# Performance work log

Hardware: AMD Instinct MI355X
Metric: run time of the kernel (lower is better)

The kernel has to match this reference:

```python
import jax, jax.numpy as jnp
import numpy as np

NUM_HEADS = 8
NUM_GROUPS = 32
EPS = 1e-5
RESCALE = 1.0


def setup_inputs() -> dict:
    key = jax.random.key(0)
    ks = jax.random.split(key, 7)
    b, c, h, w = 16, 512, 32, 32
    return {
        "x": jax.random.normal(ks[0], (b, c, h, w), jnp.float32),
        "norm_w": jax.random.normal(ks[1], (c,), jnp.float32),
        "norm_b": jax.random.normal(ks[2], (c,), jnp.float32),
        "qkv_w": jax.random.normal(ks[3], (3 * c, c), jnp.float32) * (c ** -0.5),
        "qkv_b": jax.random.normal(ks[4], (3 * c,), jnp.float32) * 0.02,
        "proj_w": jax.random.normal(ks[5], (c, c), jnp.float32) * (c ** -0.5),
        "proj_b": jax.random.normal(ks[6], (c,), jnp.float32) * 0.02,
    }


def _group_norm(x, w, b):
    # x: [B, C, L]
    B, C, L = x.shape
    g = x.reshape(B, NUM_GROUPS, (C // NUM_GROUPS) * L)
    mu = jnp.mean(g, axis=-1, keepdims=True)
    var = jnp.var(g, axis=-1, keepdims=True)
    g = (g - mu) * jax.lax.rsqrt(var + EPS)
    return g.reshape(B, C, L) * w[None, :, None] + b[None, :, None]


def reference(x, norm_w, norm_b, qkv_w, qkv_b, proj_w, proj_b):
    b, c, hh, ww = x.shape
    L = hh * ww
    H = NUM_HEADS
    ch = c // H  # head dim

    xr = x.reshape(b, c, L)
    hid = _group_norm(xr, norm_w, norm_b)

    # 1x1 conv1d == matmul over channel dim: [3c, c] @ [b, c, L]
    qkv = jnp.einsum('oc,bcl->bol', qkv_w, hid) + qkv_b[None, :, None]
    # torch: reshape(b*H, 3*ch, L).split(ch) -> per-head contiguous [q|k|v] blocks
    qkv = qkv.reshape(b, H, 3, ch, L)
    q, k, v = qkv[:, :, 0], qkv[:, :, 1], qkv[:, :, 2]  # [b, H, ch, L]

    scale = 1.0 / (ch ** 0.25)
    weight = jnp.einsum('bhct,bhcs->bhts', q * scale, k * scale)
    weight = jax.nn.softmax(weight.astype(jnp.float32), axis=-1).astype(weight.dtype)
    a = jnp.einsum('bhts,bhcs->bhct', weight, v)  # [b, H, ch, L]

    h = a.reshape(b, c, L)
    h = jnp.einsum('oc,bcl->bol', proj_w, h) + proj_b[None, :, None]
    h = h.reshape(b, c, hh, ww)
    return (x + h) / RESCALE
```

## Files before the change

kernel.cpp:

```cpp
#include <hip/hip_runtime.h>
#include <hip/hip_bf16.h>
#include <stdint.h>


using f32x4  = __attribute__((ext_vector_type(4))) float;
using bf16x8 = __attribute__((ext_vector_type(8))) __bf16;
using s8v    = __attribute__((ext_vector_type(8))) short;
using s4v    = __attribute__((ext_vector_type(4))) short;

__device__ __forceinline__ short f2bf(float f){
  union { float f; unsigned u; } c; c.f = f;
  unsigned r = (c.u + 0x7FFFu + ((c.u >> 16) & 1u)) >> 16;
  return (short)r;
}

__device__ __forceinline__ void gl_lds16(const void* g, void* l){
  __builtin_amdgcn_global_load_lds((const __attribute__((address_space(1))) void*)g,
                                   (__attribute__((address_space(3))) void*)l, 16, 0, 0);
}

__global__ void k_convw(const float* __restrict__ qw, const float* __restrict__ pw,
                        short* __restrict__ qwb, short* __restrict__ pwb){
  int i = blockIdx.x * 256 + threadIdx.x;
  if (i < 1536*512) qwb[i] = f2bf(qw[i]);
  else              pwb[i - 1536*512] = f2bf(pw[i - 1536*512]);
}

__global__ __launch_bounds__(256) void k_gnorm(const float* __restrict__ x,
                                               const float* __restrict__ w,
                                               const float* __restrict__ bia,
                                               short* __restrict__ hid){
  int b = blockIdx.x >> 5;
  int g = blockIdx.x & 31;
  int tid = threadIdx.x;
  const float* xg = x + ((size_t)b*512 + g*16)*1024;
  int l0 = tid * 4;
  float v[16][4];
  float s1 = 0.f, s2 = 0.f;
  #pragma unroll
  for (int c = 0; c < 16; c++){
    f32x4 t = *(const f32x4*)(xg + c*1024 + l0);
    #pragma unroll
    for (int j = 0; j < 4; j++){ v[c][j] = t[j]; s1 += t[j]; s2 += t[j]*t[j]; }
  }
  #pragma unroll
  for (int m = 32; m; m >>= 1){ s1 += __shfl_xor(s1, m); s2 += __shfl_xor(s2, m); }
  __shared__ float r1[4], r2[4];
  int wv = tid >> 6, ln = tid & 63;
  if (ln == 0){ r1[wv] = s1; r2[wv] = s2; }
  __syncthreads();
  s1 = r1[0]+r1[1]+r1[2]+r1[3];
  s2 = r2[0]+r2[1]+r2[2]+r2[3];
  float mu = s1 * (1.f/16384.f);
  float var = s2 * (1.f/16384.f) - mu*mu;
  float rs = rsqrtf(var + 1e-5f);
  float ww[16], bb[16];
  #pragma unroll
  for (int c = 0; c < 16; c++){ ww[c] = w[g*16+c]*rs; bb[c] = bia[g*16+c]; }
  #pragma unroll
  for (int j = 0; j < 4; j++){
    short o[16];
    #pragma unroll
    for (int c = 0; c < 16; c++) o[c] = f2bf((v[c][j]-mu)*ww[c] + bb[c]);
    short* dst = hid + ((size_t)(b*1024 + l0 + j))*512 + g*16;
    *(s8v*)dst     = *(s8v*)o;
    *(s8v*)(dst+8) = *(s8v*)(o+8);
  }
}

template<int EPI>
__global__ __launch_bounds__(256) void k_gemm(
    const short* __restrict__ A, const short* __restrict__ Bm,
    const float* __restrict__ bias, const float* __restrict__ xres,
    short* __restrict__ q_t, short* __restrict__ k_t, short* __restrict__ v_t,
    float* __restrict__ outp)
{
  __shared__ short Al[128*64];
  __shared__ short Bl[128*64];
  int m0 = blockIdx.y * 128;
  int n0 = blockIdx.x * 128;
  int tid = threadIdx.x;
  int lane = tid & 63;
  int wv = tid >> 6;
  int wr = wv >> 1, wc = wv & 1;
  f32x4 acc[4][4] = {};

  for (int k0 = 0; k0 < 512; k0 += 64){
    __syncthreads();
    #pragma unroll
    for (int i = 0; i < 8; i++){
      int cc = wv*8 + i;
      if (cc < 16){
        int slot = cc*64 + lane;
        int row = slot >> 3, off = slot & 7;
        gl_lds16(A + (size_t)(m0+row)*512 + k0 + (off ^ (row&7))*8,
                 (char*)Al + cc*1024);
      } else {
        int slot = (cc-16)*64 + lane;
        int row = slot >> 3, off = slot & 7;
        gl_lds16(Bm + (size_t)(n0+row)*512 + k0 + (off ^ (row&7))*8,
                 (char*)Bl + (cc-16)*1024);
      }
    }
    __syncthreads();
    #pragma unroll
    for (int kk = 0; kk < 2; kk++){
      bf16x8 af[4], bf[4];
      #pragma unroll
      for (int m = 0; m < 4; m++){
        int row = wr*64 + m*16 + (lane&15);
        int byte = row*128 + (((kk*64) + ((lane>>4)*16)) ^ ((row&7)<<4));
        af[m] = *(const bf16x8*)((char*)Al + byte);
      }
      #pragma unroll
      for (int n = 0; n < 4; n++){
        int row = wc*64 + n*16 + (lane&15);
        int byte = row*128 + (((kk*64) + ((lane>>4)*16)) ^ ((row&7)<<4));
        bf[n] = *(const bf16x8*)((char*)Bl + byte);
      }
      #pragma unroll
      for (int m = 0; m < 4; m++)
        #pragma unroll
        for (int n = 0; n < 4; n++)
          acc[m][n] = __builtin_amdgcn_mfma_f32_16x16x32_bf16(af[m], bf[n], acc[m][n], 0, 0, 0);
    }
  }

  if (EPI == 0){
    #pragma unroll
    for (int m = 0; m < 4; m++){
      int ob  = m0 + wr*64 + m*16 + ((lane>>4)<<2);
      int hh  = ob / 192;
      int rem = ob % 192;
      int sel = rem >> 6;
      int c0  = rem & 63;
      float bs[4];
      #pragma unroll
      for (int r = 0; r < 4; r++) bs[r] = bias[ob+r];
      #pragma unroll
      for (int n = 0; n < 4; n++){
        int nn = n0 + wc*64 + n*16 + (lane&15);
        int bb = nn >> 10, ll = nn & 1023;
        int bh = bb*8 + hh;
        if (sel == 2){
          short* dst = v_t + ((size_t)bh*64 + c0)*1024 + ll;
          #pragma unroll
          for (int r = 0; r < 4; r++) dst[r*1024] = f2bf(acc[m][n][r] + bs[r]);
        } else {
          float sc = (sel == 0) ? 0.125f : 1.0f;
          short o4[4];
          #pragma unroll
          for (int r = 0; r < 4; r++) o4[r] = f2bf((acc[m][n][r] + bs[r]) * sc);
          short* dst = (sel == 0 ? q_t : k_t) + ((size_t)bh*1024 + ll)*64 + c0;
          *(s4v*)dst = *(s4v*)o4;
        }
      }
    }
  } else {
    #pragma unroll
    for (int m = 0; m < 4; m++){
      int ob = m0 + wr*64 + m*16 + ((lane>>4)<<2);
      float bs[4];
      #pragma unroll
      for (int r = 0; r < 4; r++) bs[r] = bias[ob+r];
      #pragma unroll
      for (int n = 0; n < 4; n++){
        int nn = n0 + wc*64 + n*16 + (lane&15);
        int bb = nn >> 10, ll = nn & 1023;
        #pragma unroll
        for (int r = 0; r < 4; r++){
          size_t idx = ((size_t)bb*512 + ob + r)*1024 + ll;
          outp[idx] = xres[idx] + acc[m][n][r] + bs[r];
        }
      }
    }
  }
}

__global__ __launch_bounds__(256, 4) void k_attn(
    const short* __restrict__ q_t, const short* __restrict__ k_t,
    const short* __restrict__ v_t, short* __restrict__ a_bt)
{
  __shared__ short Kl[64*64];
  __shared__ short Vl[64*64];
  int qb = blockIdx.x;
  int hh = blockIdx.y;
  int bb = blockIdx.z;
  int bh = bb*8 + hh;
  int tid = threadIdx.x;
  int lane = tid & 63;
  int wv = tid >> 6;
  int l15 = lane & 15, g = lane >> 4;

  bf16x8 qf[2][2];
  #pragma unroll
  for (int qt = 0; qt < 2; qt++){
    const short* qbase = q_t + ((size_t)bh*1024 + qb*128 + qt*64 + wv*16 + l15)*64 + g*8;
    qf[qt][0] = *(const bf16x8*)(qbase);
    qf[qt][1] = *(const bf16x8*)(qbase + 32);
  }

  f32x4 o[2][4] = {};
  float psum[2] = {0.f, 0.f};

  for (int s0 = 0; s0 < 1024; s0 += 64){
    __syncthreads();
    #pragma unroll
    for (int i = 0; i < 4; i++){
      int cc = wv*4 + i;
      if (cc < 8){
        int slot = cc*64 + lane;
        int row = slot >> 3, off = slot & 7;
        gl_lds16(k_t + ((size_t)bh*1024 + s0 + row)*64 + (off ^ (row&7))*8,
                 (char*)Kl + cc*1024);
      } else {
        int slot = (cc-8)*64 + lane;
        int row = slot >> 3, off = slot & 7;
        gl_lds16(v_t + ((size_t)bh*64 + row)*1024 + s0 + (off ^ (row&7))*8,
                 (char*)Vl + (cc-8)*1024);
      }
    }
    __syncthreads();

    f32x4 sc[2][4] = {};
    #pragma unroll
    for (int j = 0; j < 4; j++){
      #pragma unroll
      for (int ks = 0; ks < 2; ks++){
        int row = j*16 + l15;
        int byte = row*128 + (((ks*64) + (g*16)) ^ ((row&7)<<4));
        bf16x8 kf = *(const bf16x8*)((char*)Kl + byte);
        #pragma unroll
        for (int qt = 0; qt < 2; qt++)
          sc[qt][j] = __builtin_amdgcn_mfma_f32_16x16x32_bf16(kf, qf[qt][ks], sc[qt][j], 0, 0, 0);
      }
    }

    #pragma unroll
    for (int ks = 0; ks < 2; ks++){
      bf16x8 pa[2];
      #pragma unroll
      for (int qt = 0; qt < 2; qt++){
        #pragma unroll
        for (int i2 = 0; i2 < 8; i2++){
          float e = __expf(sc[qt][2*ks + (i2>>2)][i2&3]);
          psum[qt] += e;
          pa[qt][i2] = (__bf16)e;
        }
      }
      #pragma unroll
      for (int jd = 0; jd < 4; jd++){
        int row = jd*16 + l15;
        int swz = (row&7)<<4;
        union { s4v h[2]; bf16x8 b; } vb;
        vb.h[0] = *(const s4v*)((char*)Vl + row*128 + (((ks*64) + g*8) ^ swz));
        vb.h[1] = *(const s4v*)((char*)Vl + row*128 + (((ks*64) + 32 + g*8) ^ swz));
        #pragma unroll
        for (int qt = 0; qt < 2; qt++)
          o[qt][jd] = __builtin_amdgcn_mfma_f32_16x16x32_bf16(pa[qt], vb.b, o[qt][jd], 0, 0, 0);
      }
    }
  }

  #pragma unroll
  for (int qt = 0; qt < 2; qt++){
    psum[qt] += __shfl_xor(psum[qt], 16);
    psum[qt] += __shfl_xor(psum[qt], 32);
  }
  #pragma unroll
  for (int qt = 0; qt < 2; qt++){
    #pragma unroll
    for (int r = 0; r < 4; r++){
      float lr = __shfl(psum[qt], g*4 + r);
      float inv = 1.f / lr;
      int qrow = qb*128 + qt*64 + wv*16 + g*4 + r;
      #pragma unroll
      for (int jd = 0; jd < 4; jd++)
        a_bt[((size_t)bb*1024 + qrow)*512 + hh*64 + jd*16 + l15] = f2bf(o[qt][jd][r] * inv);
    }
  }
}

extern "C" void kernel_launch(void* const* d_in, const int* in_sizes, int n_in,
                              void* d_out, int out_size, void* d_ws, size_t ws_size,
                              hipStream_t stream){
  const float* x  = (const float*)d_in[0];
  const float* nw = (const float*)d_in[1];
  const float* nb = (const float*)d_in[2];
  const float* qw = (const float*)d_in[3];
  const float* qb = (const float*)d_in[4];
  const float* pw = (const float*)d_in[5];
  const float* pb = (const float*)d_in[6];
  float* outp = (float*)d_out;

  char* ws = (char*)d_ws;
  short* hid  = (short*)(ws);
  short* qwb  = (short*)(ws + 16777216);
  short* pwb  = (short*)(ws + 18350080);
  short* q_t  = (short*)(ws + 18874368);
  short* k_t  = (short*)(ws + 35651584);
  short* v_t  = (short*)(ws + 52428800);
  short* a_bt = hid;
  if (ws_size < 69206016) return;

  k_convw<<<4096, 256, 0, stream>>>(qw, pw, qwb, pwb);
  k_gnorm<<<512, 256, 0, stream>>>(x, nw, nb, hid);
  dim3 g1(128, 12);
  k_gemm<0><<<g1, 256, 0, stream>>>(qwb, hid, qb, nullptr, q_t, k_t, v_t, nullptr);
  dim3 g2(8, 8, 16);
  k_attn<<<g2, 256, 0, stream>>>(q_t, k_t, v_t, a_bt);
  dim3 g3(128, 4);
  k_gemm<1><<<g3, 256, 0, stream>>>(pwb, a_bt, pb, x, nullptr, nullptr, nullptr, outp);
}
```

Before: 138.8 us.

## Double-buffer LDS in GEMM and attention, remap blocks per XCD, change V layout

Both the GEMM and attention kernels now double-buffer their LDS tiles. The next tile is issued with global_load_lds before computing the current one, using vmcnt waits and raw barriers, so load latency can overlap the MFMA work. Grids are flattened and remapped so blocks sharing the same B/K/V operands land on the same XCD, which should improve L2 reuse. The V tile gets a new LDS layout that matches the PV MFMA read pattern, and setprio is raised around MFMA groups. LDS use doubles, which may reduce occupancy, and the manual vmcnt counts have to match the number of loads issued.

```diff
diff --git a/kernel.cpp b/kernel.cpp
--- a/kernel.cpp
+++ b/kernel.cpp
@@ -75,18 +75,19 @@
     short* __restrict__ q_t, short* __restrict__ k_t, short* __restrict__ v_t,
     float* __restrict__ outp)
 {
-  __shared__ short Al[128*64];
-  __shared__ short Bl[128*64];
-  int m0 = blockIdx.y * 128;
-  int n0 = blockIdx.x * 128;
+  __shared__ short Al[2][128*64];
+  __shared__ short Bl[2][128*64];
+  int id = blockIdx.x;
+  int xcd = id & 7, ix = id >> 3;
+  int n0 = (xcd + 8*(ix & 15)) * 128;
+  int m0 = (ix >> 4) * 128;
   int tid = threadIdx.x;
   int lane = tid & 63;
   int wv = tid >> 6;
   int wr = wv >> 1, wc = wv & 1;
   f32x4 acc[4][4] = {};
 
-  for (int k0 = 0; k0 < 512; k0 += 64){
-    __syncthreads();
+  auto STAGE = [&](int db, int k0){
     #pragma unroll
     for (int i = 0; i < 8; i++){
       int cc = wv*8 + i;
@@ -94,15 +95,22 @@
         int slot = cc*64 + lane;
         int row = slot >> 3, off = slot & 7;
         gl_lds16(A + (size_t)(m0+row)*512 + k0 + (off ^ (row&7))*8,
-                 (char*)Al + cc*1024);
+                 (char*)Al[db] + cc*1024);
       } else {
         int slot = (cc-16)*64 + lane;
         int row = slot >> 3, off = slot & 7;
         gl_lds16(Bm + (size_t)(n0+row)*512 + k0 + (off ^ (row&7))*8,
-                 (char*)Bl + (cc-16)*1024);
-      }
-    }
-    __syncthreads();
+                 (char*)Bl[db] + (cc-16)*1024);
+      }
+    }
+  };
+
+  STAGE(0, 0);
+  for (int t = 0; t < 8; t++){
+    STAGE((t+1)&1, ((t+1)&7)*64);
+    asm volatile("s_waitcnt vmcnt(8)" ::: "memory");
+    __builtin_amdgcn_s_barrier();
+    int db = t & 1;
     #pragma unroll
     for (int kk = 0; kk < 2; kk++){
       bf16x8 af[4], bf[4];
@@ -110,20 +118,23 @@
       for (int m = 0; m < 4; m++){
         int row = wr*64 + m*16 + (lane&15);
         int byte = row*128 + (((kk*64) + ((lane>>4)*16)) ^ ((row&7)<<4));
-        af[m] = *(const bf16x8*)((char*)Al + byte);
+        af[m] = *(const bf16x8*)((char*)Al[db] + byte);
       }
       #pragma unroll
       for (int n = 0; n < 4; n++){
         int row = wc*64 + n*16 + (lane&15);
         int byte = row*128 + (((kk*64) + ((lane>>4)*16)) ^ ((row&7)<<4));
-        bf[n] = *(const bf16x8*)((char*)Bl + byte);
-      }
+        bf[n] = *(const bf16x8*)((char*)Bl[db] + byte);
+      }
+      __builtin_amdgcn_s_setprio(1);
       #pragma unroll
       for (int m = 0; m < 4; m++)
         #pragma unroll
         for (int n = 0; n < 4; n++)
           acc[m][n] = __builtin_amdgcn_mfma_f32_16x16x32_bf16(af[m], bf[n], acc[m][n], 0, 0, 0);
-    }
+      __builtin_amdgcn_s_setprio(0);
+    }
+    __builtin_amdgcn_s_barrier();
   }
 
   if (EPI == 0){
@@ -181,12 +192,13 @@
     const short* __restrict__ q_t, const short* __restrict__ k_t,
     const short* __restrict__ v_t, short* __restrict__ a_bt)
 {
-  __shared__ short Kl[64*64];
-  __shared__ short Vl[64*64];
-  int qb = blockIdx.x;
-  int hh = blockIdx.y;
-  int bb = blockIdx.z;
-  int bh = bb*8 + hh;
+  __shared__ short Kl[2][64*64];
+  __shared__ short Vl[2][64*64];
+  int id = blockIdx.x;
+  int xcd = id & 7, ix = id >> 3;
+  int bh = xcd*16 + (ix >> 3);
+  int qb = ix & 7;
+  int bb = bh >> 3, hh = bh & 7;
   int tid = threadIdx.x;
   int lane = tid & 63;
   int wv = tid >> 6;
@@ -199,12 +211,9 @@
     qf[qt][0] = *(const bf16x8*)(qbase);
     qf[qt][1] = *(const bf16x8*)(qbase + 32);
   }
-
-  f32x4 o[2][4] = {};
-  float psum[2] = {0.f, 0.f};
-
-  for (int s0 = 0; s0 < 1024; s0 += 64){
-    __syncthreads();
+  asm volatile("" :: "v"(qf[0][0]), "v"(qf[0][1]), "v"(qf[1][0]), "v"(qf[1][1]));
+
+  auto STAGE = [&](int db, int s0){
     #pragma unroll
     for (int i = 0; i < 4; i++){
       int cc = wv*4 + i;
@@ -212,15 +221,27 @@
         int slot = cc*64 + lane;
         int row = slot >> 3, off = slot & 7;
         gl_lds16(k_t + ((size_t)bh*1024 + s0 + row)*64 + (off ^ (row&7))*8,
-                 (char*)Kl + cc*1024);
+                 (char*)Kl[db] + cc*1024);
       } else {
-        int slot = (cc-8)*64 + lane;
-        int row = slot >> 3, off = slot & 7;
-        gl_lds16(v_t + ((size_t)bh*64 + row)*1024 + s0 + (off ^ (row&7))*8,
-                 (char*)Vl + (cc-8)*1024);
-      }
-    }
-    __syncthreads();
+        int lam = (cc-8)*1024 + lane*16;
+        int sblk = lam >> 11;
+        int d    = (lam >> 5) & 63;
+        int inn  = (lam & 31) >> 1;
+        gl_lds16(v_t + ((size_t)bh*64 + d)*1024 + s0 + sblk*16 + inn,
+                 (char*)Vl[db] + (cc-8)*1024);
+      }
+    }
+  };
+
+  f32x4 o[2][4] = {};
+  float psum[2] = {0.f, 0.f};
+
+  STAGE(0, 0);
+  for (int t = 0; t < 16; t++){
+    STAGE((t+1)&1, ((t+1)&15)*64);
+    asm volatile("s_waitcnt vmcnt(4)" ::: "memory");
+    __builtin_amdgcn_s_barrier();
+    int db = t & 1;
 
     f32x4 sc[2][4] = {};
     #pragma unroll
@@ -229,10 +250,12 @@
       for (int ks = 0; ks < 2; ks++){
         int row = j*16 + l15;
         int byte = row*128 + (((ks*64) + (g*16)) ^ ((row&7)<<4));
-        bf16x8 kf = *(const bf16x8*)((char*)Kl + byte);
+        bf16x8 kf = *(const bf16x8*)((char*)Kl[db] + byte);
+        __builtin_amdgcn_s_setprio(1);
         #pragma unroll
         for (int qt = 0; qt < 2; qt++)
           sc[qt][j] = __builtin_amdgcn_mfma_f32_16x16x32_bf16(kf, qf[qt][ks], sc[qt][j], 0, 0, 0);
+        __builtin_amdgcn_s_setprio(0);
       }
     }
 
@@ -250,16 +273,18 @@
       }
       #pragma unroll
       for (int jd = 0; jd < 4; jd++){
-        int row = jd*16 + l15;
-        int swz = (row&7)<<4;
+        int d = jd*16 + l15;
         union { s4v h[2]; bf16x8 b; } vb;
-        vb.h[0] = *(const s4v*)((char*)Vl + row*128 + (((ks*64) + g*8) ^ swz));
-        vb.h[1] = *(const s4v*)((char*)Vl + row*128 + (((ks*64) + 32 + g*8) ^ swz));
+        vb.h[0] = *(const s4v*)((char*)Vl[db] + (2*ks+0)*2048 + d*32 + g*8);
+        vb.h[1] = *(const s4v*)((char*)Vl[db] + (2*ks+1)*2048 + d*32 + g*8);
+        __builtin_amdgcn_s_setprio(1);
         #pragma unroll
         for (int qt = 0; qt < 2; qt++)
           o[qt][jd] = __builtin_amdgcn_mfma_f32_16x16x32_bf16(pa[qt], vb.b, o[qt][jd], 0, 0, 0);
-      }
-    }
+        __builtin_amdgcn_s_setprio(0);
+      }
+    }
+    __builtin_amdgcn_s_barrier();
   }
 
   #pragma unroll
@@ -305,10 +330,7 @@
 
   k_convw<<<4096, 256, 0, stream>>>(qw, pw, qwb, pwb);
   k_gnorm<<<512, 256, 0, stream>>>(x, nw, nb, hid);
-  dim3 g1(128, 12);
-  k_gemm<0><<<g1, 256, 0, stream>>>(qwb, hid, qb, nullptr, q_t, k_t, v_t, nullptr);
-  dim3 g2(8, 8, 16);
-  k_attn<<<g2, 256, 0, stream>>>(q_t, k_t, v_t, a_bt);
-  dim3 g3(128, 4);
-  k_gemm<1><<<g3, 256, 0, stream>>>(pwb, a_bt, pb, x, nullptr, nullptr, nullptr, outp);
-}
+  k_gemm<0><<<1536, 256, 0, stream>>>(qwb, hid, qb, nullptr, q_t, k_t, v_t, nullptr);
+  k_attn<<<1024, 256, 0, stream>>>(q_t, k_t, v_t, a_bt);
+  k_gemm<1><<<512, 256, 0, stream>>>(pwb, a_bt, pb, x, nullptr, nullptr, nullptr, outp);
+}
```

Result: no change. 138.1 us (-0.5%).
